# Optimization experiments

Measured on AMD Instinct MI355X. Metric: run time of the kernel, lower is better.

The kernel has to match this reference:

```python
import jax, jax.numpy as jnp
import numpy as np

EPS = 1e-5

def conv2d(x, w, b, groups=1):
    out = jax.lax.conv_general_dilated(
        x, w, (1, 1), 'SAME',
        dimension_numbers=('NCHW', 'OIHW', 'NCHW'),
        feature_group_count=groups)
    return out + b[None, :, None, None]

def bilinear_gather(img, ys, xs):
    # img [B,C,H,W]; ys,xs [B,K,H,W] float sample coords; zero padding outside
    H, W = img.shape[2], img.shape[3]
    y0 = jnp.floor(ys)
    x0 = jnp.floor(xs)
    wy = ys - y0
    wx = xs - x0

    def corner(yi, xi, w):
        valid = (yi >= 0) & (yi <= H - 1) & (xi >= 0) & (xi <= W - 1)
        yc = jnp.clip(yi, 0, H - 1).astype(jnp.int32)
        xc = jnp.clip(xi, 0, W - 1).astype(jnp.int32)
        # gather -> [B,C,K,H,W]
        v = jax.vmap(lambda im, y, x: im[:, y, x])(img, yc, xc)
        return v * (w * valid)[:, None]

    return (corner(y0, x0, (1 - wy) * (1 - wx))
            + corner(y0, x0 + 1, (1 - wy) * wx)
            + corner(y0 + 1, x0, wy * (1 - wx))
            + corner(y0 + 1, x0 + 1, wy * wx))

def deform_conv(x, offset, w, b):
    # torchvision DeformConv2d, kernel 3x3, stride 1, pad 1; offset layout [B,2*K,H,W] as (dy,dx) per tap
    B, C, H, W = x.shape
    K = 9
    ky = (jnp.repeat(jnp.arange(3), 3) - 1).astype(x.dtype)  # [9]
    kx = (jnp.tile(jnp.arange(3), 3) - 1).astype(x.dtype)
    off = offset.reshape(B, K, 2, H, W)
    base_y = jnp.arange(H, dtype=x.dtype)[None, None, :, None]
    base_x = jnp.arange(W, dtype=x.dtype)[None, None, None, :]
    ys = base_y + ky[None, :, None, None] + off[:, :, 0]  # [B,K,H,W]
    xs = base_x + kx[None, :, None, None] + off[:, :, 1]
    sampled = bilinear_gather(x, ys, xs)                  # [B,C,K,H,W]
    out = jnp.einsum('bckhw,ock->bohw', sampled, w.reshape(w.shape[0], C, K))
    return out + b[None, :, None, None]

def setup_inputs() -> dict:
    key = jax.random.key(0)
    ks = jax.random.split(key, 12)
    C, O = 128, 128
    B, H, W = 4, 96, 96
    s = 0.05
    return {
        'x': jax.random.normal(ks[0], (B, C, H, W), jnp.float32),
        'dw_w': jax.random.normal(ks[1], (C, 1, 3, 3), jnp.float32) * s,
        'dw_b': jax.random.normal(ks[2], (C,), jnp.float32) * s,
        'pw_w': jax.random.normal(ks[3], (O, C, 1, 1), jnp.float32) * s,
        'pw_b': jax.random.normal(ks[4], (O,), jnp.float32) * s,
        'off_w': jax.random.normal(ks[5], (18, O, 3, 3), jnp.float32) * s,
        'off_b': jax.random.normal(ks[6], (18,), jnp.float32) * s,
        'dc_w': jax.random.normal(ks[7], (O, O, 3, 3), jnp.float32) * s,
        'dc_b': jax.random.normal(ks[8], (O,), jnp.float32) * s,
        'ln_g': jnp.ones((O,), jnp.float32),
        'ln_b': jnp.zeros((O,), jnp.float32),
    }

def reference(x, dw_w, dw_b, pw_w, pw_b, off_w, off_b, dc_w, dc_b, ln_g, ln_b):
    C = x.shape[1]
    # depthwise-separable conv
    h = conv2d(x, dw_w, dw_b, groups=C)
    h = conv2d(h, pw_w, pw_b)
    # InstanceNorm2d (affine=False)
    mu = h.mean((2, 3), keepdims=True)
    var = h.var((2, 3), keepdims=True)
    dsc = (h - mu) * jax.lax.rsqrt(var + EPS)
    # Dropout2d: inference mode -> identity
    offset = conv2d(dsc, off_w, off_b)              # [B,18,H,W]
    dc = deform_conv(dsc, offset, dc_w, dc_b)       # [B,O,H,W]
    # LayerNorm over channels (NHWC last axis)
    nhwc = dc.transpose(0, 2, 3, 1)
    m = nhwc.mean(-1, keepdims=True)
    v = nhwc.var(-1, keepdims=True)
    ln = (nhwc - m) * jax.lax.rsqrt(v + EPS) * ln_g + ln_b
    attn = jax.nn.sigmoid(ln.transpose(0, 3, 1, 2))
    return dsc * attn
```

## Files before the change

### kernel.cpp

```cpp
#include <hip/hip_runtime.h>
#include <math.h>

#define HW 9216
#define WD 96
#define NC 128

typedef unsigned short u16;
typedef __attribute__((ext_vector_type(8))) short short8;
typedef __attribute__((ext_vector_type(4))) float v4f;

__device__ __forceinline__ int rfl(int v){ return __builtin_amdgcn_readfirstlane(v); }
__device__ __forceinline__ float bu2f(u16 s){ return __uint_as_float(((unsigned)s)<<16); }
__device__ __forceinline__ u16 f2b(float f){ unsigned u = __float_as_uint(f);
  return (u16)((u + 0x7fffu + ((u>>16)&1u))>>16); }

__global__ __launch_bounds__(256) void prep_weights(const float* __restrict__ pw_w,
    const float* __restrict__ off_w, const float* __restrict__ dc_w,
    u16* __restrict__ wpwb, u16* __restrict__ wob, u16* __restrict__ wdcb){
  int t = blockIdx.x*256 + threadIdx.x;
  if (t < 16384) wpwb[t] = f2b(pw_w[t]);
  if (t < 36864){
    int ntl = t/18432, rem = t - ntl*18432;
    int s = rem>>9, l = (rem>>3)&63, e = rem&7;
    int o = ntl*16 + (l&15);
    int c = (s&3)*32 + ((l>>4)<<3) + e;
    int k = s>>2;
    wob[t] = (o<18) ? f2b(off_w[(o*128+c)*9+k]) : (u16)0;
  }
  if (t < 147456){
    int e = t&7, l = (t>>3)&63, f = (t>>9)&7, g = t>>12;
    int s = g%18, r = g/18;
    int nt = f>>1, ks = f&1;
    int c = ((s&1)<<6) + ks*32 + ((l>>4)<<3) + e;
    int o = (r<<6) + nt*16 + (l&15);
    int k = s>>1;
    wdcb[t] = f2b(dc_w[(o*128+c)*9 + k]);
  }
}

__global__ __launch_bounds__(256) void dw_conv(const float* __restrict__ x,
    const float* __restrict__ w, const float* __restrict__ bias, float* __restrict__ h1){
  int n = blockIdx.x*256 + threadIdx.x;
  int bc = rfl(n / 2304);
  int qp = n - bc*2304;
  int p = qp*4;
  int c = bc & 127;
  int yy = p / WD, xx = p - yy*WD;
  const float* xc = x + (size_t)bc*HW;
  const float* wc = w + c*9;
  float bs = bias[c];
  float a0=bs, a1=bs, a2=bs, a3=bs;
  #pragma unroll
  for (int r=0;r<3;r++){
    int y2 = yy + r - 1;
    if (y2>=0 && y2<96){
      const float* row = xc + y2*WD + xx;
      float4 vc = *(const float4*)row;
      float vl = (xx>0)  ? row[-1] : 0.f;
      float vr = (xx<92) ? row[4]  : 0.f;
      float w0 = wc[r*3+0], w1 = wc[r*3+1], w2 = wc[r*3+2];
      a0 = fmaf(w0, vl,   fmaf(w1, vc.x, fmaf(w2, vc.y, a0)));
      a1 = fmaf(w0, vc.x, fmaf(w1, vc.y, fmaf(w2, vc.z, a1)));
      a2 = fmaf(w0, vc.y, fmaf(w1, vc.z, fmaf(w2, vc.w, a2)));
      a3 = fmaf(w0, vc.z, fmaf(w1, vc.w, fmaf(w2, vr,   a3)));
    }
  }
  *(float4*)(h1 + (size_t)bc*HW + p) = make_float4(a0,a1,a2,a3);
}

__global__ __launch_bounds__(256) void pw_mfma(const float* __restrict__ h1,
    const u16* __restrict__ wpwb, const float* __restrict__ pw_b, float* __restrict__ h2){
  __shared__ short Aw[128*136];
  __shared__ short Bw[128*68];
  int blk = blockIdx.x; int row0 = blk*64;
  int b = rfl(row0/HW); int pbase = rfl(row0 - b*HW);
  int t = threadIdx.x;
  #pragma unroll
  for (int i=0;i<8;i++){
    int idx = i*256 + t; int o = idx>>4, seg = idx&15;
    *(short8*)&Aw[o*136 + seg*8] = *(const short8*)(wpwb + o*128 + seg*8);
  }
  #pragma unroll
  for (int i=0;i<8;i++){
    int idx = i*256 + t; int c = idx>>4, seg = idx&15;
    float4 v = *(const float4*)(h1 + (size_t)(b*NC+c)*HW + pbase + seg*4);
    ushort4 pk = make_ushort4(f2b(v.x), f2b(v.y), f2b(v.z), f2b(v.w));
    *(ushort4*)&Bw[c*68 + seg*4] = pk;
  }
  __syncthreads();
  int w = rfl(t>>6); int l = t&63; int q = l>>4; int ln = l&15;
  v4f acc[8];
  #pragma unroll
  for (int mt=0;mt<8;mt++) acc[mt] = (v4f){0.f,0.f,0.f,0.f};
  #pragma unroll
  for (int ks=0;ks<4;ks++){
    short8 bf;
    #pragma unroll
    for (int j=0;j<8;j++) bf[j] = Bw[(ks*32 + q*8 + j)*68 + w*16 + ln];
    #pragma unroll
    for (int mt=0;mt<8;mt++){
      short8 af = *(short8*)&Aw[(mt*16+ln)*136 + ks*32 + q*8];
      acc[mt] = __builtin_amdgcn_mfma_f32_16x16x32_bf16(af, bf, acc[mt], 0,0,0);
    }
  }
  int px = pbase + w*16 + ln;
  #pragma unroll
  for (int mt=0;mt<8;mt++){
    #pragma unroll
    for (int r=0;r<4;r++){
      int o = mt*16 + q*4 + r;
      h2[(size_t)(b*NC+o)*HW + px] = acc[mt][r] + pw_b[o];
    }
  }
}

__global__ __launch_bounds__(256) void inorm_stats(const float* __restrict__ h2, float* __restrict__ st){
  int bc = blockIdx.x;
  const float* src = h2 + (size_t)bc*HW;
  float s=0.f, ss=0.f;
  for (int i=threadIdx.x; i<HW; i+=256){ float v=src[i]; s+=v; ss=fmaf(v,v,ss); }
  #pragma unroll
  for (int off=32; off; off>>=1){ s += __shfl_down(s,off); ss += __shfl_down(ss,off); }
  __shared__ float rsm[2][4];
  int wave = threadIdx.x>>6, lane = threadIdx.x&63;
  if (lane==0){ rsm[0][wave]=s; rsm[1][wave]=ss; }
  __syncthreads();
  if (threadIdx.x==0){
    float S = rsm[0][0]+rsm[0][1]+rsm[0][2]+rsm[0][3];
    float SS= rsm[1][0]+rsm[1][1]+rsm[1][2]+rsm[1][3];
    float mu = S * (1.f/9216.f);
    float var = SS * (1.f/9216.f) - mu*mu;
    st[bc*2]   = mu;
    st[bc*2+1] = rsqrtf(var + 1e-5f);
  }
}

__global__ __launch_bounds__(256) void make_dsc(const float* __restrict__ h2,
    const float* __restrict__ st, float* __restrict__ dsc,
    u16* __restrict__ dscT, u16* __restrict__ dscL){
  int blk = blockIdx.x;
  int pt = blk % 144; int r = blk/144; int ch = r & 1; int b = r >> 1;
  int c0 = ch*64, pbase = pt*64;
  __shared__ float tile[64][65];
  int tr = threadIdx.x >> 2;
  int g  = threadIdx.x & 3;
  int c  = c0 + tr;
  float mu = st[(b*128+c)*2];
  float rs = st[(b*128+c)*2+1];
  const float* src = h2 + (size_t)(b*128+c)*HW + pbase + g*16;
  float* d = dsc + (size_t)(b*128+c)*HW + pbase + g*16;
  #pragma unroll
  for (int i=0;i<4;i++){
    float4 v = *(const float4*)(src + i*4);
    v.x=(v.x-mu)*rs; v.y=(v.y-mu)*rs; v.z=(v.z-mu)*rs; v.w=(v.w-mu)*rs;
    *(float4*)(d + i*4) = v;
    tile[tr][g*16+i*4+0]=v.x; tile[tr][g*16+i*4+1]=v.y;
    tile[tr][g*16+i*4+2]=v.z; tile[tr][g*16+i*4+3]=v.w;
  }
  __syncthreads();
  int pr = tr;
  u16* dt = dscT + ((size_t)b*HW + pbase + pr)*NC + c0 + g*16;
  u16* dl = dscL + ((size_t)b*HW + pbase + pr)*NC + c0 + g*16;
  #pragma unroll
  for (int i=0;i<4;i++){
    float v0 = tile[g*16+i*4+0][pr], v1 = tile[g*16+i*4+1][pr];
    float v2 = tile[g*16+i*4+2][pr], v3 = tile[g*16+i*4+3][pr];
    ushort4 hi = make_ushort4(f2b(v0), f2b(v1), f2b(v2), f2b(v3));
    ushort4 lo = make_ushort4(f2b(v0-bu2f(hi.x)), f2b(v1-bu2f(hi.y)),
                              f2b(v2-bu2f(hi.z)), f2b(v3-bu2f(hi.w)));
    *(ushort4*)(dt + i*4) = hi;
    *(ushort4*)(dl + i*4) = lo;
  }
}

__global__ __launch_bounds__(256) void off_mfma(const u16* __restrict__ dscT,
    const u16* __restrict__ dscL, const u16* __restrict__ wobp,
    const float* __restrict__ off_b, float4* __restrict__ wg, ushort4* __restrict__ ad){
  __shared__ short As[2][2][32*40];
  __shared__ float Po[18*32];
  int blk = blockIdx.x;
  int tile = (blk&7)*144 + (blk>>3);
  int row0 = tile*32;
  int b = rfl(row0/HW); int pbase = rfl(row0 - b*HW);
  int t = threadIdx.x;
  int apx = t>>3, hl = (t>>2)&1, segA = t&3;
  int w = rfl(t>>6); int l = t&63; int q = l>>4; int ln = l&15;
  int mt = w&1, ntl = w>>1;
  int P = pbase + apx;
  int py = P/96, px_ = P - 96*(P/96);
  const u16* gsrc = (hl ? dscL : dscT) + (size_t)b*HW*NC;
  const u16* wbase = wobp + ntl*18432 + l*8;
  uint4 rgA, rgB; short8 bregE, bregO;
  auto issue = [&](int s, uint4& rg){
    int k = s>>2, cseg = s&3;
    int y2 = py + k/3 - 1, x2 = px_ + k%3 - 1;
    bool valid = ((unsigned)y2 < 96u) && ((unsigned)x2 < 96u);
    int off = ((y2*96 + x2)*NC) + cseg*32 + segA*8;
    rg = valid ? *(const uint4*)(gsrc + off) : (uint4){0,0,0,0};
  };
  auto issueB = [&](int s)->short8{
    return *(const short8*)(wbase + s*512);
  };
  auto commit = [&](int buf, uint4& rg){
    *(short8*)&As[buf][hl][apx*40 + segA*8] = *(short8*)&rg;
  };
  v4f acc = (v4f){0.f,0.f,0.f,0.f};
  auto step = [&](int buf, short8 bf){
    short8 ah = *(short8*)&As[buf][0][(mt*16+ln)*40 + q*8];
    short8 al = *(short8*)&As[buf][1][(mt*16+ln)*40 + q*8];
    acc = __builtin_amdgcn_mfma_f32_16x16x32_bf16(ah, bf, acc, 0,0,0);
    acc = __builtin_amdgcn_mfma_f32_16x16x32_bf16(al, bf, acc, 0,0,0);
  };
  issue(0, rgA); issue(1, rgB);
  bregE = issueB(0); bregO = issueB(1);
  commit(0, rgA);
  __syncthreads();
  #pragma unroll 1
  for (int s=0;s<36;s+=2){
    if (s+2<36) issue(s+2, rgA);
    commit(1, rgB);
    step(0, bregE);
    if (s+2<36) bregE = issueB(s+2);
    __syncthreads();
    if (s+3<36) issue(s+3, rgB);
    if (s+2<36) commit(0, rgA);
    step(1, bregO);
    if (s+3<36) bregO = issueB(s+3);
    __syncthreads();
  }
  int o = ntl*16 + ln;
  if (o < 18){
    float ob = off_b[o];
    #pragma unroll
    for (int r=0;r<4;r++) Po[o*32 + mt*16 + q*4 + r] = acc[r] + ob;
  }
  __syncthreads();
  #pragma unroll
  for (int i=0;i<2;i++){
    int idx = i*256 + t;
    if (idx < 288){
      int pxl = idx & 31, k = idx >> 5;
      int Pp = pbase + pxl;
      float dy = Po[(2*k)*32 + pxl], dx = Po[(2*k+1)*32 + pxl];
      float ys = (float)(Pp/96 + k/3 - 1) + dy;
      float xs = (float)(Pp%96 + k%3 - 1) + dx;
      float fy0 = floorf(ys), fx0 = floorf(xs);
      float wy = ys - fy0, wx = xs - fx0;
      int y0 = (int)fy0, x0 = (int)fx0;
      int y1 = y0+1, x1 = x0+1;
      float vy0 = (y0>=0 && y0<=95) ? 1.f : 0.f;
      float vy1 = (y1>=0 && y1<=95) ? 1.f : 0.f;
      float vx0 = (x0>=0 && x0<=95) ? 1.f : 0.f;
      float vx1 = (x1>=0 && x1<=95) ? 1.f : 0.f;
      int y0c=min(max(y0,0),95), y1c=min(max(y1,0),95);
      int x0c=min(max(x0,0),95), x1c=min(max(x1,0),95);
      float4 w4;
      w4.x = (1.f-wy)*(1.f-wx)*vy0*vx0;
      w4.y = (1.f-wy)*wx*vy0*vx1;
      w4.z = wy*(1.f-wx)*vy1*vx0;
      w4.w = wy*wx*vy1*vx1;
      int gi = (b*9 + k)*HW + pbase + pxl;
      wg[gi] = w4;
      ad[gi] = make_ushort4((u16)(y0c*WD+x0c), (u16)(y0c*WD+x1c),
                            (u16)(y1c*WD+x0c), (u16)(y1c*WD+x1c));
    }
  }
}

__global__ __launch_bounds__(256) void deform_mfma(const u16* __restrict__ dscT,
    const u16* __restrict__ wdcb, const float* __restrict__ dc_b,
    const float4* __restrict__ wg, const ushort4* __restrict__ ad,
    float* __restrict__ dc_t){
  __shared__ short As[2][32*68];
  __shared__ float4 WgL[288];
  __shared__ ushort4 AdL[288];
  int blk = blockIdx.x;
  int tile = (blk&7)*144 + (blk>>3);
  int row0 = tile*32;
  int b = rfl(row0/HW); int pbase = rfl(row0 - b*HW);
  int t = threadIdx.x;
  int apx = t>>3, cs8 = t&7;
  int w = rfl(t>>6); int l = t&63; int q = l>>4; int ln = l&15;
  int mt = w&1, nb = (w>>1)*4, rrole = rfl(w>>1);
  const u16* db0 = dscT + (size_t)b*HW*NC + cs8*8;
  const u16* wbase = wdcb + (size_t)rrole*(18*4096) + l*8;
  #pragma unroll
  for (int i=0;i<2;i++){
    int idx = i*256 + t;
    if (idx < 288){ int k = idx>>5, pxl = idx&31; int gi = (b*9+k)*HW + pbase + pxl;
      WgL[idx] = wg[gi]; AdL[idx] = ad[gi]; }
  }
  __syncthreads();
  uint4 gA0,gA1,gA2,gA3, gB0,gB1,gB2,gB3;
  float4 wvA, wvB;
  short8 bregE[8], bregO[8];
  auto issueG = [&](int s, float4& wv, uint4& r0, uint4& r1, uint4& r2, uint4& r3){
    int k = s>>1, cb = (s&1)<<6;
    ushort4 av = AdL[k*32+apx]; wv = WgL[k*32+apx];
    const u16* db = db0 + cb;
    r0 = *(const uint4*)(db + (int)av.x*NC);
    r1 = *(const uint4*)(db + (int)av.y*NC);
    r2 = *(const uint4*)(db + (int)av.z*NC);
    r3 = *(const uint4*)(db + (int)av.w*NC);
  };
  auto issueB = [&](int s, short8* dst){
    const u16* p = wbase + s*4096;
    #pragma unroll
    for (int f=0;f<8;f++) dst[f] = *(const short8*)(p + f*512);
  };
  auto commitA = [&](int buf, float4 wv, uint4& r0, uint4& r1, uint4& r2, uint4& r3){
    const u16* pa=(const u16*)&r0; const u16* pb=(const u16*)&r1;
    const u16* pc=(const u16*)&r2; const u16* pd=(const u16*)&r3;
    short8 sv;
    #pragma unroll
    for (int j=0;j<8;j++){
      float f = wv.x*bu2f(pa[j]) + wv.y*bu2f(pb[j]) + wv.z*bu2f(pc[j]) + wv.w*bu2f(pd[j]);
      sv[j] = (short)f2b(f);
    }
    *(short8*)&As[buf][apx*68 + cs8*8] = sv;
  };
  v4f acc[4];
  #pragma unroll
  for (int nt=0;nt<4;nt++) acc[nt] = (v4f){0.f,0.f,0.f,0.f};
  auto step = [&](int buf, const short8* bb){
    #pragma unroll
    for (int ks=0;ks<2;ks++){
      short8 af = *(const short8*)&As[buf][(mt*16+ln)*68 + ks*32 + q*8];
      #pragma unroll
      for (int nt=0;nt<4;nt++)
        acc[nt] = __builtin_amdgcn_mfma_f32_16x16x32_bf16(af, bb[nt*2+ks], acc[nt], 0,0,0);
    }
  };
  issueG(0, wvA, gA0,gA1,gA2,gA3); issueB(0, bregE);
  issueG(1, wvB, gB0,gB1,gB2,gB3); issueB(1, bregO);
  commitA(0, wvA, gA0,gA1,gA2,gA3);
  __syncthreads();
  #pragma unroll 1
  for (int s=0;s<18;s+=2){
    if (s+2<18) issueG(s+2, wvA, gA0,gA1,gA2,gA3);
    commitA(1, wvB, gB0,gB1,gB2,gB3);
    step(0, bregE);
    if (s+2<18) issueB(s+2, bregE);
    __syncthreads();
    if (s+3<18) issueG(s+3, wvB, gB0,gB1,gB2,gB3);
    if (s+2<18) commitA(0, wvA, gA0,gA1,gA2,gA3);
    step(1, bregO);
    if (s+3<18) issueB(s+3, bregO);
    __syncthreads();
  }
  #pragma unroll
  for (int nt=0;nt<4;nt++){
    int o = (nb+nt)*16 + ln;
    float bias = dc_b[o];
    #pragma unroll
    for (int r=0;r<4;r++){
      int px = pbase + mt*16 + q*4 + r;
      dc_t[((size_t)b*HW + px)*NC + o] = acc[nt][r] + bias;
    }
  }
}

__global__ __launch_bounds__(256) void epilogue(const float* __restrict__ dc_t,
    const float* __restrict__ dsc, const float* __restrict__ ln_g,
    const float* __restrict__ ln_b, float* __restrict__ out){
  __shared__ float T[64*129];
  __shared__ float Ps[4*64], Qs[4*64], Ms[64], Rs[64];
  int blk = blockIdx.x;
  int b = rfl(blk/144); int pbase = rfl(blk - (blk/144)*144)*64;
  int t = threadIdx.x;
  #pragma unroll
  for (int i=0;i<8;i++){
    int idx = i*256 + t; int px = idx>>5, seg = idx&31;
    float4 v = *(const float4*)(dc_t + ((size_t)b*HW + pbase + px)*NC + seg*4);
    float* d = &T[px*129 + seg*4];
    d[0]=v.x; d[1]=v.y; d[2]=v.z; d[3]=v.w;
  }
  __syncthreads();
  int px = t&63, cg = t>>6;
  float s=0.f, ss=0.f;
  #pragma unroll
  for (int i=0;i<32;i++){ float v = T[px*129 + cg*32 + i]; s += v; ss = fmaf(v,v,ss); }
  Ps[cg*64+px] = s; Qs[cg*64+px] = ss;
  __syncthreads();
  if (t<64){
    float S = Ps[px]+Ps[64+px]+Ps[128+px]+Ps[192+px];
    float SS= Qs[px]+Qs[64+px]+Qs[128+px]+Qs[192+px];
    float m = S*(1.f/128.f);
    float var = SS*(1.f/128.f) - m*m;
    Ms[px] = m; Rs[px] = rsqrtf(var + 1e-5f);
  }
  __syncthreads();
  float m = Ms[px], rs = Rs[px];
  #pragma unroll 4
  for (int i=0;i<32;i++){
    int c = cg*32 + i;
    float ln = (T[px*129+c] - m)*rs*ln_g[c] + ln_b[c];
    float attn = 1.f/(1.f+__expf(-ln));
    size_t idx = (size_t)(b*NC+c)*HW + pbase + px;
    out[idx] = dsc[idx]*attn;
  }
}

extern "C" void kernel_launch(void* const* d_in, const int* in_sizes, int n_in,
                              void* d_out, int out_size, void* d_ws, size_t ws_size,
                              hipStream_t stream){
  const float* x    = (const float*)d_in[0];
  const float* dw_w = (const float*)d_in[1];
  const float* dw_b = (const float*)d_in[2];
  const float* pw_w = (const float*)d_in[3];
  const float* pw_b = (const float*)d_in[4];
  const float* off_w= (const float*)d_in[5];
  const float* off_b= (const float*)d_in[6];
  const float* dc_w = (const float*)d_in[7];
  const float* dc_b = (const float*)d_in[8];
  const float* ln_g = (const float*)d_in[9];
  const float* ln_b = (const float*)d_in[10];
  float* out = (float*)d_out;

  float* W    = (float*)d_ws;
  float*   bufA = W;
  float*   bufB = W + 4718592;
  u16*     dscT = (u16*)(W + 9437184);
  u16*     dscL = (u16*)(W + 11796480);
  float4*  wg   = (float4*)(W + 14155776);
  ushort4* ad   = (ushort4*)(W + 15482880);
  float*   st   = W + 16146432;
  u16*     wpwb = (u16*)(W + 16147456);
  u16*     wob  = (u16*)(W + 16155648);
  u16*     wdcb = (u16*)(W + 16174080);

  prep_weights<<<576, 256, 0, stream>>>(pw_w, off_w, dc_w, wpwb, wob, wdcb);
  dw_conv     <<<4608, 256, 0, stream>>>(x, dw_w, dw_b, bufA);
  pw_mfma     <<<576, 256, 0, stream>>>(bufA, wpwb, pw_b, bufB);
  inorm_stats <<<512, 256, 0, stream>>>(bufB, st);
  make_dsc    <<<1152, 256, 0, stream>>>(bufB, st, bufA, dscT, dscL);
  off_mfma    <<<1152, 256, 0, stream>>>(dscT, dscL, wob, off_b, wg, ad);
  deform_mfma <<<1152, 256, 0, stream>>>(dscT, wdcb, dc_b, wg, ad, bufB);
  epilogue    <<<576, 256, 0, stream>>>(bufB, bufA, ln_g, ln_b, out);
}
```

Before: 205.7 us.

## Fuse channel LayerNorm, sigmoid gating epilogue into deform MFMA kernel

Moves the per-pixel LayerNorm over channels, the sigmoid and the multiply by dsc into the tail of the deformable-conv MFMA kernel. Row statistics are reduced with lane shuffles across the 16-lane groups and combined across the two waves through a small shared array. This removes the separate epilogue launch and the write and re-read of the 4.7M-float dc_t intermediate. In exchange it adds register pressure and a barrier at the end of the MFMA kernel, and its output stores are narrower float4 segments.

After: 198.9 us. 3.3% less time.

```diff
diff --git a/kernel.cpp b/kernel.cpp
--- a/kernel.cpp
+++ b/kernel.cpp
@@ -270,10 +270,12 @@
 __global__ __launch_bounds__(256) void deform_mfma(const u16* __restrict__ dscT,
     const u16* __restrict__ wdcb, const float* __restrict__ dc_b,
     const float4* __restrict__ wg, const ushort4* __restrict__ ad,
-    float* __restrict__ dc_t){
+    const float* __restrict__ dsc, const float* __restrict__ ln_g,
+    const float* __restrict__ ln_b, float* __restrict__ out){
   __shared__ short As[2][32*68];
   __shared__ float4 WgL[288];
   __shared__ ushort4 AdL[288];
+  __shared__ float RS[2][4][4][4];
   int blk = blockIdx.x;
   int tile = (blk&7)*144 + (blk>>3);
   int row0 = tile*32;
@@ -348,56 +350,57 @@
     if (s+3<18) issueB(s+3, bregO);
     __syncthreads();
   }
+  int o_[4]; float bias_[4], g_[4], bb_[4];
   #pragma unroll
   for (int nt=0;nt<4;nt++){
     int o = (nb+nt)*16 + ln;
-    float bias = dc_b[o];
+    o_[nt] = o; bias_[nt] = dc_b[o]; g_[nt] = ln_g[o]; bb_[nt] = ln_b[o];
+  }
+  float s_[4] = {0.f,0.f,0.f,0.f}, ss_[4] = {0.f,0.f,0.f,0.f};
+  #pragma unroll
+  for (int r=0;r<4;r++){
+    #pragma unroll
+    for (int nt=0;nt<4;nt++){
+      float v = acc[nt][r] + bias_[nt];
+      s_[r] += v; ss_[r] = fmaf(v, v, ss_[r]);
+    }
+  }
+  #pragma unroll
+  for (int off=1; off<16; off<<=1){
     #pragma unroll
     for (int r=0;r<4;r++){
-      int px = pbase + mt*16 + q*4 + r;
-      dc_t[((size_t)b*HW + px)*NC + o] = acc[nt][r] + bias;
-    }
-  }
-}
-
-__global__ __launch_bounds__(256) void epilogue(const float* __restrict__ dc_t,
-    const float* __restrict__ dsc, const float* __restrict__ ln_g,
-    const float* __restrict__ ln_b, float* __restrict__ out){
-  __shared__ float T[64*129];
-  __shared__ float Ps[4*64], Qs[4*64], Ms[64], Rs[64];
-  int blk = blockIdx.x;
-  int b = rfl(blk/144); int pbase = rfl(blk - (blk/144)*144)*64;
-  int t = threadIdx.x;
-  #pragma unroll
-  for (int i=0;i<8;i++){
-    int idx = i*256 + t; int px = idx>>5, seg = idx&31;
-    float4 v = *(const float4*)(dc_t + ((size_t)b*HW + pbase + px)*NC + seg*4);
-    float* d = &T[px*129 + seg*4];
-    d[0]=v.x; d[1]=v.y; d[2]=v.z; d[3]=v.w;
-  }
-  __syncthreads();
-  int px = t&63, cg = t>>6;
-  float s=0.f, ss=0.f;
-  #pragma unroll
-  for (int i=0;i<32;i++){ float v = T[px*129 + cg*32 + i]; s += v; ss = fmaf(v,v,ss); }
-  Ps[cg*64+px] = s; Qs[cg*64+px] = ss;
-  __syncthreads();
-  if (t<64){
-    float S = Ps[px]+Ps[64+px]+Ps[128+px]+Ps[192+px];
-    float SS= Qs[px]+Qs[64+px]+Qs[128+px]+Qs[192+px];
+      s_[r]  += __shfl_xor(s_[r],  off);
+      ss_[r] += __shfl_xor(ss_[r], off);
+    }
+  }
+  if (ln==0){
+    #pragma unroll
+    for (int r=0;r<4;r++){ RS[0][w][q][r] = s_[r]; RS[1][w][q][r] = ss_[r]; }
+  }
+  __syncthreads();
+  float m_[4], rs_[4];
+  #pragma unroll
+  for (int r=0;r<4;r++){
+    float S  = RS[0][w][q][r] + RS[0][w^2][q][r];
+    float SS = RS[1][w][q][r] + RS[1][w^2][q][r];
     float m = S*(1.f/128.f);
     float var = SS*(1.f/128.f) - m*m;
-    Ms[px] = m; Rs[px] = rsqrtf(var + 1e-5f);
-  }
-  __syncthreads();
-  float m = Ms[px], rs = Rs[px];
-  #pragma unroll 4
-  for (int i=0;i<32;i++){
-    int c = cg*32 + i;
-    float ln = (T[px*129+c] - m)*rs*ln_g[c] + ln_b[c];
-    float attn = 1.f/(1.f+__expf(-ln));
-    size_t idx = (size_t)(b*NC+c)*HW + pbase + px;
-    out[idx] = dsc[idx]*attn;
+    m_[r] = m; rs_[r] = rsqrtf(var + 1e-5f);
+  }
+  int pxb = pbase + mt*16 + q*4;
+  #pragma unroll
+  for (int nt=0;nt<4;nt++){
+    size_t base = (size_t)(b*NC + o_[nt])*HW + pxb;
+    float4 dv = *(const float4*)(dsc + base);
+    float4 ov;
+    #pragma unroll
+    for (int r=0;r<4;r++){
+      float v = acc[nt][r] + bias_[nt];
+      float lnv = (v - m_[r])*rs_[r]*g_[nt] + bb_[nt];
+      float attn = 1.f/(1.f+__expf(-lnv));
+      ((float*)&ov)[r] = ((const float*)&dv)[r] * attn;
+    }
+    *(float4*)(out + base) = ov;
   }
 }
 
@@ -435,6 +438,5 @@
   inorm_stats <<<512, 256, 0, stream>>>(bufB, st);
   make_dsc    <<<1152, 256, 0, stream>>>(bufB, st, bufA, dscT, dscL);
   off_mfma    <<<1152, 256, 0, stream>>>(dscT, dscL, wob, off_b, wg, ad);
-  deform_mfma <<<1152, 256, 0, stream>>>(dscT, wdcb, dc_b, wg, ad, bufB);
-  epilogue    <<<576, 256, 0, stream>>>(bufB, bufA, ln_g, ln_b, out);
-}
+  deform_mfma <<<1152, 256, 0, stream>>>(dscT, wdcb, dc_b, wg, ad, bufA, ln_g, ln_b, out);
+}
```
